# Kernel tuning notes

Measured on AMD Instinct MI355X. Metric: run time of the kernel, lower is better.

The kernel has to match this reference:

```python
import jax, jax.numpy as jnp
import numpy as np
import math

B, S, D, H = 2, 2048, 1024, 16
DK = D // H


def setup_inputs() -> dict:
    key = jax.random.key(0)
    ks = jax.random.split(key, 11)
    s = 1.0 / math.sqrt(D)
    return {
        "q": jax.random.normal(ks[0], (B, S, D), jnp.float32),
        "k": jax.random.normal(ks[1], (B, S, D), jnp.float32),
        "v": jax.random.normal(ks[2], (B, S, D), jnp.float32),
        "Wq": jax.random.normal(ks[3], (D, D), jnp.float32) * s,
        "bq": jnp.zeros((D,), jnp.float32),
        "Wk": jax.random.normal(ks[4], (D, D), jnp.float32) * s,
        "bk": jnp.zeros((D,), jnp.float32),
        "Wv": jax.random.normal(ks[5], (D, D), jnp.float32) * s,
        "bv": jnp.zeros((D,), jnp.float32),
        "Wo": jax.random.normal(ks[6], (D, D), jnp.float32) * s,
        "bo": jnp.zeros((D,), jnp.float32),
        "mask": jnp.ones((B, 1, S), dtype=bool),
    }


def reference(q, k, v, Wq, bq, Wk, bk, Wv, bv, Wo, bo, mask):
    # project and split heads: [B,S,D] -> [B,H,S,DK]
    def proj(x, W, b):
        return (x @ W.T + b).reshape(B, S, H, DK).transpose(0, 2, 1, 3)

    qh, kh, vh = proj(q, Wq, bq), proj(k, Wk, bk), proj(v, Wv, bv)
    scores = jnp.einsum("bhqd,bhkd->bhqk", qh, kh) / math.sqrt(DK)
    # 3D mask [B,1,S], self-attn: expand to [B,1,S,S] via outer AND
    m = mask[:, :, None, :] & mask[:, :, :, None]
    scores = jnp.where(m, scores, -1e9)
    attn = jax.nn.softmax(scores, axis=-1)
    attn = jnp.nan_to_num(attn, nan=0.0, posinf=0.0, neginf=0.0)
    out = jnp.einsum("bhqk,bhkd->bhqd", attn, vh)  # [B,H,S,DK]
    concat = out.transpose(0, 2, 1, 3).reshape(B, S, D)
    return concat @ Wo.T + bo
```

## Files before the change

### kernel.cpp

```cpp
#include <hip/hip_runtime.h>
#include <hip/hip_bf16.h>
#include <stdint.h>

using bf16 = __bf16;
typedef __attribute__((ext_vector_type(8))) __bf16 bf16x8;
typedef __attribute__((ext_vector_type(4))) float f32x4;

typedef const __attribute__((address_space(1))) void* gptr_t;
typedef __attribute__((address_space(3))) void* lptr_t;

__device__ __forceinline__ void gld16(const void* g, void* l) {
    __builtin_amdgcn_global_load_lds((gptr_t)g, (lptr_t)l, 16, 0, 0);
}

__global__ __launch_bounds__(256)
void cvt_kern(const float* __restrict__ in, bf16* __restrict__ out, int n)
{
    const int i = (blockIdx.x * 256 + threadIdx.x) * 8;
    if (i >= n) return;
    const float4 f0 = *(const float4*)(in + i);
    const float4 f1 = *(const float4*)(in + i + 4);
    bf16x8 v = { (bf16)f0.x, (bf16)f0.y, (bf16)f0.z, (bf16)f0.w,
                 (bf16)f1.x, (bf16)f1.y, (bf16)f1.z, (bf16)f1.w };
    *(bf16x8*)(out + i) = v;
}

template<int MODE, bool XWS, bool OUTF32>
__global__ __launch_bounds__(512, 2)
void gemm_mfma(const void* __restrict__ Xv, const bf16* __restrict__ W,
               const float* __restrict__ bias, void* __restrict__ Yv)
{
    constexpr int K = 1024, N = 1024;
    constexpr int NT = K / 64;
    __shared__ bf16 As[2][128 * 64];
    __shared__ bf16 Bs[2][128 * 64];

    const int t = threadIdx.x;
    const int w = t >> 6, lane = t & 63, quad = lane >> 4, l15 = lane & 15;
    const int m0 = blockIdx.y * 128, n0 = blockIdx.x * 128;
    const int wm = (w >> 1) * 32, wn = (w & 1) * 64;

    const int srow = t >> 3;
    const int sseg = (t & 7) ^ (srow & 7);

    const float* Xf   = (const float*)Xv;
    const bf16*  gA16 = (const bf16*)Xv + (size_t)(m0 + srow) * K + sseg * 8;
    const bf16*  gB   = W + (size_t)(n0 + srow) * K + sseg * 8;

    f32x4 acc[2][4] = {};

    if constexpr (XWS) {
        gld16(gA16,          &As[0][t * 8]);
        gld16(gA16 + 64 * K, &As[0][t * 8 + 4096]);
    } else {
        #pragma unroll
        for (int r = 0; r < 2; ++r) {
            const int g = r * 512 + t;
            const int row = g >> 3, sg = g & 7;
            const float* p = Xf + (size_t)(m0 + row) * K + sg * 8;
            const float4 f0 = *(const float4*)p;
            const float4 f1 = *(const float4*)(p + 4);
            bf16x8 vv = { (bf16)f0.x, (bf16)f0.y, (bf16)f0.z, (bf16)f0.w,
                          (bf16)f1.x, (bf16)f1.y, (bf16)f1.z, (bf16)f1.w };
            *(bf16x8*)&As[0][row * 64 + ((sg ^ (row & 7)) * 8)] = vv;
        }
    }
    gld16(gB,          &Bs[0][t * 8]);
    gld16(gB + 64 * K, &Bs[0][t * 8 + 4096]);
    __syncthreads();

    #pragma unroll 2
    for (int kk = 0; kk < NT; ++kk) {
        const int cur = kk & 1;
        const int kn = (kk + 1) * 64;

        float4 pf0[2], pf1[2];
        if (kk + 1 < NT) {
            if constexpr (XWS) {
                gld16(gA16 + kn,          &As[cur ^ 1][t * 8]);
                gld16(gA16 + kn + 64 * K, &As[cur ^ 1][t * 8 + 4096]);
            } else {
                #pragma unroll
                for (int r = 0; r < 2; ++r) {
                    const int g = r * 512 + t;
                    const int row = g >> 3, sg = g & 7;
                    const float* p = Xf + (size_t)(m0 + row) * K + kn + sg * 8;
                    pf0[r] = *(const float4*)p;
                    pf1[r] = *(const float4*)(p + 4);
                }
            }
            gld16(gB + kn,          &Bs[cur ^ 1][t * 8]);
            gld16(gB + kn + 64 * K, &Bs[cur ^ 1][t * 8 + 4096]);
        }

        bf16x8 af[2][2], bfr[4][2];
        #pragma unroll
        for (int mt = 0; mt < 2; ++mt)
            #pragma unroll
            for (int kt = 0; kt < 2; ++kt) {
                const int row = wm + mt * 16 + l15;
                const int seg = (kt * 4 + quad) ^ (row & 7);
                af[mt][kt] = *(const bf16x8*)&As[cur][row * 64 + seg * 8];
            }
        #pragma unroll
        for (int nt = 0; nt < 4; ++nt)
            #pragma unroll
            for (int kt = 0; kt < 2; ++kt) {
                const int row = wn + nt * 16 + l15;
                const int seg = (kt * 4 + quad) ^ (row & 7);
                bfr[nt][kt] = *(const bf16x8*)&Bs[cur][row * 64 + seg * 8];
            }
        #pragma unroll
        for (int kt = 0; kt < 2; ++kt)
            #pragma unroll
            for (int mt = 0; mt < 2; ++mt)
                #pragma unroll
                for (int nt = 0; nt < 4; ++nt)
                    acc[mt][nt] = __builtin_amdgcn_mfma_f32_16x16x32_bf16(
                        af[mt][kt], bfr[nt][kt], acc[mt][nt], 0, 0, 0);

        if (kk + 1 < NT) {
            if constexpr (!XWS) {
                #pragma unroll
                for (int r = 0; r < 2; ++r) {
                    const int g = r * 512 + t;
                    const int row = g >> 3, sg = g & 7;
                    bf16x8 vv = { (bf16)pf0[r].x, (bf16)pf0[r].y,
                                  (bf16)pf0[r].z, (bf16)pf0[r].w,
                                  (bf16)pf1[r].x, (bf16)pf1[r].y,
                                  (bf16)pf1[r].z, (bf16)pf1[r].w };
                    *(bf16x8*)&As[cur ^ 1][row * 64 + ((sg ^ (row & 7)) * 8)] = vv;
                }
            }
        }
        __syncthreads();
    }

    #pragma unroll
    for (int nt = 0; nt < 4; ++nt) {
        const int col = n0 + wn + nt * 16 + l15;
        const float bv = bias[col];
        #pragma unroll
        for (int mt = 0; mt < 2; ++mt)
            #pragma unroll
            for (int i = 0; i < 4; ++i) {
                const int row = m0 + wm + mt * 16 + quad * 4 + i;
                const float v = acc[mt][nt][i] + bv;
                if (MODE == 0) {
                    const size_t off = (size_t)row * N + col;
                    if (OUTF32) ((float*)Yv)[off] = v;
                    else        ((bf16*)Yv)[off]  = (bf16)v;
                } else {
                    const int b = row >> 11, s = row & 2047;
                    const int h = col >> 6, d = col & 63;
                    ((bf16*)Yv)[(((size_t)(b * 16 + h) * 64 + d) << 11) + s] = (bf16)v;
                }
            }
    }
}

__global__ __launch_bounds__(512, 4)
void attn_mfma(const bf16* __restrict__ Q, const bf16* __restrict__ Kg,
               const bf16* __restrict__ Vt, bf16* Cc)
{
    constexpr int S = 2048, D = 1024, DK = 64, LDP = 72;
    __shared__ bf16 Qs[128 * 64];
    __shared__ bf16 Ks[64 * 64];
    __shared__ bf16 Vs[80 * 64];
    __shared__ bf16 Ps[8][16 * LDP];

    const int t = threadIdx.x;
    const int w = t >> 6, lane = t & 63, quad = lane >> 4, l15 = lane & 15;
    const int bh = blockIdx.y, b = bh >> 4, h = bh & 15;
    const int q0 = blockIdx.x * 128;
    const int wq = w * 16;

    const int srow = t >> 3;
    const int sseg = (t & 7) ^ (srow & 7);

    for (int i = t; i < 16 * 64; i += 512) {
        const int r = 64 + (i >> 6);
        Vs[r * 64 + (i & 63)] = (r == 64) ? (bf16)1.0f : (bf16)0.0f;
    }

    {
        const bf16* gQ = Q + (size_t)(b * S + q0 + srow) * D + h * DK + sseg * 8;
        gld16(gQ,                  Qs + t * 8);
        gld16(gQ + (size_t)64 * D, Qs + t * 8 + 4096);
    }
    __syncthreads();

    bf16x8 aq[2];
    #pragma unroll
    for (int kt = 0; kt < 2; ++kt) {
        const int row = wq + l15;
        const int seg = (kt * 4 + quad) ^ (row & 7);
        aq[kt] = *(const bf16x8*)&Qs[row * 64 + seg * 8];
    }

    f32x4 o[5] = {};
    float mrow[4];
    #pragma unroll
    for (int i = 0; i < 4; ++i) mrow[i] = -1e30f;

    const float c = 0.125f * 1.44269504088896340736f;

    const bf16* gK = Kg + (size_t)(b * S + srow) * D + h * DK + sseg * 8;
    const bf16* gV = Vt + ((size_t)bh * DK + srow) * S + sseg * 8;

    for (int s0 = 0; s0 < S; s0 += 64) {
        gld16(gK + (size_t)s0 * D, Ks + t * 8);
        gld16(gV + s0,             Vs + t * 8);
        __syncthreads();

        f32x4 sa[4] = {};
        bf16x8 bk[4][2];
        #pragma unroll
        for (int nt = 0; nt < 4; ++nt)
            #pragma unroll
            for (int kt = 0; kt < 2; ++kt) {
                const int row = nt * 16 + l15;
                const int seg = (kt * 4 + quad) ^ (row & 7);
                bk[nt][kt] = *(const bf16x8*)&Ks[row * 64 + seg * 8];
            }
        #pragma unroll
        for (int kt = 0; kt < 2; ++kt)
            #pragma unroll
            for (int nt = 0; nt < 4; ++nt)
                sa[nt] = __builtin_amdgcn_mfma_f32_16x16x32_bf16(
                    aq[kt], bk[nt][kt], sa[nt], 0, 0, 0);

        #pragma unroll
        for (int i = 0; i < 4; ++i) {
            float v = fmaxf(fmaxf(sa[0][i], sa[1][i]),
                            fmaxf(sa[2][i], sa[3][i])) * c;
            v = fmaxf(v, __shfl_xor(v, 1));
            v = fmaxf(v, __shfl_xor(v, 2));
            v = fmaxf(v, __shfl_xor(v, 4));
            v = fmaxf(v, __shfl_xor(v, 8));
            if (__any(v > mrow[i] + 8.0f)) {
                const float mnew = fmaxf(mrow[i], v);
                const float alpha = __builtin_amdgcn_exp2f(mrow[i] - mnew);
                mrow[i] = mnew;
                #pragma unroll
                for (int nt = 0; nt < 5; ++nt)
                    o[nt][i] *= alpha;
            }
            const int prow = quad * 4 + i;
            #pragma unroll
            for (int nt = 0; nt < 4; ++nt) {
                const float pv = __builtin_amdgcn_exp2f(sa[nt][i] * c - mrow[i]);
                Ps[w][prow * LDP + nt * 16 + l15] = (bf16)pv;
            }
        }

        bf16x8 ap[2], bvv[5][2];
        #pragma unroll
        for (int kt = 0; kt < 2; ++kt)
            ap[kt] = *(const bf16x8*)&Ps[w][l15 * LDP + kt * 32 + quad * 8];
        #pragma unroll
        for (int nt = 0; nt < 5; ++nt)
            #pragma unroll
            for (int kt = 0; kt < 2; ++kt) {
                const int row = nt * 16 + l15;
                const int seg = (kt * 4 + quad) ^ (row & 7);
                bvv[nt][kt] = *(const bf16x8*)&Vs[row * 64 + seg * 8];
            }
        #pragma unroll
        for (int kt = 0; kt < 2; ++kt)
            #pragma unroll
            for (int nt = 0; nt < 5; ++nt)
                o[nt] = __builtin_amdgcn_mfma_f32_16x16x32_bf16(
                    ap[kt], bvv[nt][kt], o[nt], 0, 0, 0);

        __syncthreads();
    }

    #pragma unroll
    for (int i = 0; i < 4; ++i) {
        const int row = q0 + wq + quad * 4 + i;
        const float lsum = __shfl(o[4][i], quad << 4);
        const float inv = 1.0f / lsum;
        #pragma unroll
        for (int nt = 0; nt < 4; ++nt) {
            const int col = nt * 16 + l15;
            Cc[(size_t)(b * S + row) * D + h * DK + col] = (bf16)(o[nt][i] * inv);
        }
    }
}

extern "C" void kernel_launch(void* const* d_in, const int* in_sizes, int n_in,
                              void* d_out, int out_size, void* d_ws, size_t ws_size,
                              hipStream_t stream)
{
    int iq=0, ik=1, iv=2, iWq=3, ibq=4, iWk=5, ibk=6, iWv=7, ibv=8, iWo=9, ibo=10;
    if (n_in >= 12 && in_sizes[0] == 1048576) {
        iWk=0; iWo=1; iWq=2; iWv=3; ibk=4; ibo=5; ibq=6; ibv=7; ik=8; iq=10; iv=11;
    }

    const float* q  = (const float*)d_in[iq];
    const float* k  = (const float*)d_in[ik];
    const float* v  = (const float*)d_in[iv];
    const float* Wq = (const float*)d_in[iWq];
    const float* bq = (const float*)d_in[ibq];
    const float* Wk = (const float*)d_in[iWk];
    const float* bk = (const float*)d_in[ibk];
    const float* Wv = (const float*)d_in[iWv];
    const float* bv = (const float*)d_in[ibv];
    const float* Wo = (const float*)d_in[iWo];
    const float* bo = (const float*)d_in[ibo];

    bf16* Qp  = (bf16*)d_ws;
    bf16* Kp  = Qp  + (size_t)4194304;
    bf16* Vtp = Kp  + (size_t)4194304;
    bf16* Wqb = Vtp + (size_t)4194304;
    bf16* Wkb = Wqb + (size_t)1048576;
    bf16* Wvb = Wkb + (size_t)1048576;
    bf16* Wob = Wvb + (size_t)1048576;
    bf16* qb  = Wob + (size_t)1048576;
    bf16* kb  = qb  + (size_t)4194304;
    bf16* vb  = kb  + (size_t)4194304;
    bf16* Cc  = Qp;

    constexpr int WN = 1048576, XN = 4194304;
    cvt_kern<<<WN / 2048, 256, 0, stream>>>(Wq, Wqb, WN);
    cvt_kern<<<WN / 2048, 256, 0, stream>>>(Wk, Wkb, WN);
    cvt_kern<<<WN / 2048, 256, 0, stream>>>(Wv, Wvb, WN);
    cvt_kern<<<WN / 2048, 256, 0, stream>>>(Wo, Wob, WN);

    const bool pre = ws_size >= (size_t)56 * 1024 * 1024;
    dim3 gg(8, 32), bb(512);
    if (pre) {
        cvt_kern<<<XN / 2048, 256, 0, stream>>>(q, qb, XN);
        cvt_kern<<<XN / 2048, 256, 0, stream>>>(k, kb, XN);
        cvt_kern<<<XN / 2048, 256, 0, stream>>>(v, vb, XN);
        gemm_mfma<0, true, false><<<gg, bb, 0, stream>>>(qb, Wqb, bq, Qp);
        gemm_mfma<0, true, false><<<gg, bb, 0, stream>>>(kb, Wkb, bk, Kp);
        gemm_mfma<1, true, false><<<gg, bb, 0, stream>>>(vb, Wvb, bv, Vtp);
    } else {
        gemm_mfma<0, false, false><<<gg, bb, 0, stream>>>(q, Wqb, bq, Qp);
        gemm_mfma<0, false, false><<<gg, bb, 0, stream>>>(k, Wkb, bk, Kp);
        gemm_mfma<1, false, false><<<gg, bb, 0, stream>>>(v, Wvb, bv, Vtp);
    }
    attn_mfma<<<dim3(16, 32), dim3(512), 0, stream>>>(Qp, Kp, Vtp, Cc);
    gemm_mfma<0, true, true><<<gg, bb, 0, stream>>>(Cc, Wob, bo, d_out);
}
```

Measured before the change: 286.4 us.

## Rewrite bf16 GEMM with 256-thread blocks, 4x4 warp tiles and vmcnt-based pipelining

Replaces the bf16-input GEMM with a 256-thread variant in which each wave computes a 64x64 tile, so the same 128x128 block tile is covered by fewer waves with more MFMA work each. Tiles are prefetched two stages ahead with direct-to-LDS loads, and explicit s_waitcnt vmcnt plus raw barriers take the place of __syncthreads, letting loads stay in flight across iterations. Input conversion reuses a single bf16 scratch buffer interleaved with each projection, which lowers the workspace threshold for the precision-converted path. The cost is higher register pressure from 16 accumulator tiles per wave and fragile manual wait counts.

```diff
diff --git a/kernel.cpp b/kernel.cpp
--- a/kernel.cpp
+++ b/kernel.cpp
@@ -25,77 +25,51 @@
     *(bf16x8*)(out + i) = v;
 }
 
-template<int MODE, bool XWS, bool OUTF32>
-__global__ __launch_bounds__(512, 2)
-void gemm_mfma(const void* __restrict__ Xv, const bf16* __restrict__ W,
-               const float* __restrict__ bias, void* __restrict__ Yv)
+template<int MODE, bool OUTF32>
+__global__ __launch_bounds__(256, 2)
+void gemm_cnt(const bf16* __restrict__ X, const bf16* __restrict__ W,
+              const float* __restrict__ bias, void* __restrict__ Yv)
 {
-    constexpr int K = 1024, N = 1024;
-    constexpr int NT = K / 64;
+    constexpr int K = 1024, N = 1024, NT = K / 64;
     __shared__ bf16 As[2][128 * 64];
     __shared__ bf16 Bs[2][128 * 64];
 
     const int t = threadIdx.x;
     const int w = t >> 6, lane = t & 63, quad = lane >> 4, l15 = lane & 15;
     const int m0 = blockIdx.y * 128, n0 = blockIdx.x * 128;
-    const int wm = (w >> 1) * 32, wn = (w & 1) * 64;
+    const int wm = (w >> 1) * 64, wn = (w & 1) * 64;
 
     const int srow = t >> 3;
     const int sseg = (t & 7) ^ (srow & 7);
 
-    const float* Xf   = (const float*)Xv;
-    const bf16*  gA16 = (const bf16*)Xv + (size_t)(m0 + srow) * K + sseg * 8;
-    const bf16*  gB   = W + (size_t)(n0 + srow) * K + sseg * 8;
-
-    f32x4 acc[2][4] = {};
-
-    if constexpr (XWS) {
-        gld16(gA16,          &As[0][t * 8]);
-        gld16(gA16 + 64 * K, &As[0][t * 8 + 4096]);
-    } else {
-        #pragma unroll
-        for (int r = 0; r < 2; ++r) {
-            const int g = r * 512 + t;
-            const int row = g >> 3, sg = g & 7;
-            const float* p = Xf + (size_t)(m0 + row) * K + sg * 8;
-            const float4 f0 = *(const float4*)p;
-            const float4 f1 = *(const float4*)(p + 4);
-            bf16x8 vv = { (bf16)f0.x, (bf16)f0.y, (bf16)f0.z, (bf16)f0.w,
-                          (bf16)f1.x, (bf16)f1.y, (bf16)f1.z, (bf16)f1.w };
-            *(bf16x8*)&As[0][row * 64 + ((sg ^ (row & 7)) * 8)] = vv;
-        }
-    }
-    gld16(gB,          &Bs[0][t * 8]);
-    gld16(gB + 64 * K, &Bs[0][t * 8 + 4096]);
-    __syncthreads();
-
-    #pragma unroll 2
+    const bf16* gA = X + (size_t)(m0 + srow) * K + sseg * 8;
+    const bf16* gB = W + (size_t)(n0 + srow) * K + sseg * 8;
+
+    auto stage = [&](int buf, int k0) {
+        #pragma unroll
+        for (int r = 0; r < 4; ++r)
+            gld16(gA + k0 + r * 32 * K, &As[buf][t * 8 + r * 2048]);
+        #pragma unroll
+        for (int r = 0; r < 4; ++r)
+            gld16(gB + k0 + r * 32 * K, &Bs[buf][t * 8 + r * 2048]);
+    };
+
+    stage(0, 0);
+    stage(1, 64);
+
+    f32x4 acc[4][4] = {};
+
+    #pragma unroll 1
     for (int kk = 0; kk < NT; ++kk) {
         const int cur = kk & 1;
-        const int kn = (kk + 1) * 64;
-
-        float4 pf0[2], pf1[2];
-        if (kk + 1 < NT) {
-            if constexpr (XWS) {
-                gld16(gA16 + kn,          &As[cur ^ 1][t * 8]);
-                gld16(gA16 + kn + 64 * K, &As[cur ^ 1][t * 8 + 4096]);
-            } else {
-                #pragma unroll
-                for (int r = 0; r < 2; ++r) {
-                    const int g = r * 512 + t;
-                    const int row = g >> 3, sg = g & 7;
-                    const float* p = Xf + (size_t)(m0 + row) * K + kn + sg * 8;
-                    pf0[r] = *(const float4*)p;
-                    pf1[r] = *(const float4*)(p + 4);
-                }
-            }
-            gld16(gB + kn,          &Bs[cur ^ 1][t * 8]);
-            gld16(gB + kn + 64 * K, &Bs[cur ^ 1][t * 8 + 4096]);
-        }
-
-        bf16x8 af[2][2], bfr[4][2];
-        #pragma unroll
-        for (int mt = 0; mt < 2; ++mt)
+        if (kk == NT - 1) asm volatile("s_waitcnt vmcnt(0)" ::: "memory");
+        else              asm volatile("s_waitcnt vmcnt(8)" ::: "memory");
+        __builtin_amdgcn_s_barrier();
+        asm volatile("" ::: "memory");
+
+        bf16x8 af[4][2], bfr[4][2];
+        #pragma unroll
+        for (int mt = 0; mt < 4; ++mt)
             #pragma unroll
             for (int kt = 0; kt < 2; ++kt) {
                 const int row = wm + mt * 16 + l15;
@@ -113,27 +87,16 @@
         #pragma unroll
         for (int kt = 0; kt < 2; ++kt)
             #pragma unroll
-            for (int mt = 0; mt < 2; ++mt)
+            for (int mt = 0; mt < 4; ++mt)
                 #pragma unroll
                 for (int nt = 0; nt < 4; ++nt)
                     acc[mt][nt] = __builtin_amdgcn_mfma_f32_16x16x32_bf16(
                         af[mt][kt], bfr[nt][kt], acc[mt][nt], 0, 0, 0);
 
-        if (kk + 1 < NT) {
-            if constexpr (!XWS) {
-                #pragma unroll
-                for (int r = 0; r < 2; ++r) {
-                    const int g = r * 512 + t;
-                    const int row = g >> 3, sg = g & 7;
-                    bf16x8 vv = { (bf16)pf0[r].x, (bf16)pf0[r].y,
-                                  (bf16)pf0[r].z, (bf16)pf0[r].w,
-                                  (bf16)pf1[r].x, (bf16)pf1[r].y,
-                                  (bf16)pf1[r].z, (bf16)pf1[r].w };
-                    *(bf16x8*)&As[cur ^ 1][row * 64 + ((sg ^ (row & 7)) * 8)] = vv;
-                }
-            }
-        }
-        __syncthreads();
+        asm volatile("" ::: "memory");
+        __builtin_amdgcn_s_barrier();
+        asm volatile("" ::: "memory");
+        if (kk + 2 < NT) stage(cur, (kk + 2) * 64);
     }
 
     #pragma unroll
@@ -141,7 +104,7 @@
         const int col = n0 + wn + nt * 16 + l15;
         const float bv = bias[col];
         #pragma unroll
-        for (int mt = 0; mt < 2; ++mt)
+        for (int mt = 0; mt < 4; ++mt)
             #pragma unroll
             for (int i = 0; i < 4; ++i) {
                 const int row = m0 + wm + mt * 16 + quad * 4 + i;
@@ -150,6 +113,123 @@
                     const size_t off = (size_t)row * N + col;
                     if (OUTF32) ((float*)Yv)[off] = v;
                     else        ((bf16*)Yv)[off]  = (bf16)v;
+                } else {
+                    const int b = row >> 11, s = row & 2047;
+                    const int h = col >> 6, d = col & 63;
+                    ((bf16*)Yv)[(((size_t)(b * 16 + h) * 64 + d) << 11) + s] = (bf16)v;
+                }
+            }
+    }
+}
+
+template<int MODE>
+__global__ __launch_bounds__(512, 2)
+void gemm_f32(const float* __restrict__ Xf, const bf16* __restrict__ W,
+              const float* __restrict__ bias, void* __restrict__ Yv)
+{
+    constexpr int K = 1024, N = 1024;
+    constexpr int NT = K / 64;
+    __shared__ bf16 As[2][128 * 64];
+    __shared__ bf16 Bs[2][128 * 64];
+
+    const int t = threadIdx.x;
+    const int w = t >> 6, lane = t & 63, quad = lane >> 4, l15 = lane & 15;
+    const int m0 = blockIdx.y * 128, n0 = blockIdx.x * 128;
+    const int wm = (w >> 1) * 32, wn = (w & 1) * 64;
+
+    const int srow = t >> 3;
+    const int sseg = (t & 7) ^ (srow & 7);
+
+    const bf16* gB = W + (size_t)(n0 + srow) * K + sseg * 8;
+
+    f32x4 acc[2][4] = {};
+
+    #pragma unroll
+    for (int r = 0; r < 2; ++r) {
+        const int g = r * 512 + t;
+        const int row = g >> 3, sg = g & 7;
+        const float* p = Xf + (size_t)(m0 + row) * K + sg * 8;
+        const float4 f0 = *(const float4*)p;
+        const float4 f1 = *(const float4*)(p + 4);
+        bf16x8 vv = { (bf16)f0.x, (bf16)f0.y, (bf16)f0.z, (bf16)f0.w,
+                      (bf16)f1.x, (bf16)f1.y, (bf16)f1.z, (bf16)f1.w };
+        *(bf16x8*)&As[0][row * 64 + ((sg ^ (row & 7)) * 8)] = vv;
+    }
+    gld16(gB,          &Bs[0][t * 8]);
+    gld16(gB + 64 * K, &Bs[0][t * 8 + 4096]);
+    __syncthreads();
+
+    for (int kk = 0; kk < NT; ++kk) {
+        const int cur = kk & 1;
+        const int kn = (kk + 1) * 64;
+
+        float4 pf0[2], pf1[2];
+        if (kk + 1 < NT) {
+            #pragma unroll
+            for (int r = 0; r < 2; ++r) {
+                const int g = r * 512 + t;
+                const int row = g >> 3, sg = g & 7;
+                const float* p = Xf + (size_t)(m0 + row) * K + kn + sg * 8;
+                pf0[r] = *(const float4*)p;
+                pf1[r] = *(const float4*)(p + 4);
+            }
+            gld16(gB + kn,          &Bs[cur ^ 1][t * 8]);
+            gld16(gB + kn + 64 * K, &Bs[cur ^ 1][t * 8 + 4096]);
+        }
+
+        bf16x8 af[2][2], bfr[4][2];
+        #pragma unroll
+        for (int mt = 0; mt < 2; ++mt)
+            #pragma unroll
+            for (int kt = 0; kt < 2; ++kt) {
+                const int row = wm + mt * 16 + l15;
+                const int seg = (kt * 4 + quad) ^ (row & 7);
+                af[mt][kt] = *(const bf16x8*)&As[cur][row * 64 + seg * 8];
+            }
+        #pragma unroll
+        for (int nt = 0; nt < 4; ++nt)
+            #pragma unroll
+            for (int kt = 0; kt < 2; ++kt) {
+                const int row = wn + nt * 16 + l15;
+                const int seg = (kt * 4 + quad) ^ (row & 7);
+                bfr[nt][kt] = *(const bf16x8*)&Bs[cur][row * 64 + seg * 8];
+            }
+        #pragma unroll
+        for (int kt = 0; kt < 2; ++kt)
+            #pragma unroll
+            for (int mt = 0; mt < 2; ++mt)
+                #pragma unroll
+                for (int nt = 0; nt < 4; ++nt)
+                    acc[mt][nt] = __builtin_amdgcn_mfma_f32_16x16x32_bf16(
+                        af[mt][kt], bfr[nt][kt], acc[mt][nt], 0, 0, 0);
+
+        if (kk + 1 < NT) {
+            #pragma unroll
+            for (int r = 0; r < 2; ++r) {
+                const int g = r * 512 + t;
+                const int row = g >> 3, sg = g & 7;
+                bf16x8 vv = { (bf16)pf0[r].x, (bf16)pf0[r].y,
+                              (bf16)pf0[r].z, (bf16)pf0[r].w,
+                              (bf16)pf1[r].x, (bf16)pf1[r].y,
+                              (bf16)pf1[r].z, (bf16)pf1[r].w };
+                *(bf16x8*)&As[cur ^ 1][row * 64 + ((sg ^ (row & 7)) * 8)] = vv;
+            }
+        }
+        __syncthreads();
+    }
+
+    #pragma unroll
+    for (int nt = 0; nt < 4; ++nt) {
+        const int col = n0 + wn + nt * 16 + l15;
+        const float bv = bias[col];
+        #pragma unroll
+        for (int mt = 0; mt < 2; ++mt)
+            #pragma unroll
+            for (int i = 0; i < 4; ++i) {
+                const int row = m0 + wm + mt * 16 + quad * 4 + i;
+                const float v = acc[mt][nt][i] + bv;
+                if (MODE == 0) {
+                    ((bf16*)Yv)[(size_t)row * N + col] = (bf16)v;
                 } else {
                     const int b = row >> 11, s = row & 2047;
                     const int h = col >> 6, d = col & 63;
@@ -317,9 +397,7 @@
     bf16* Wkb = Wqb + (size_t)1048576;
     bf16* Wvb = Wkb + (size_t)1048576;
     bf16* Wob = Wvb + (size_t)1048576;
-    bf16* qb  = Wob + (size_t)1048576;
-    bf16* kb  = qb  + (size_t)4194304;
-    bf16* vb  = kb  + (size_t)4194304;
+    bf16* xb  = Wob + (size_t)1048576;
     bf16* Cc  = Qp;
 
     constexpr int WN = 1048576, XN = 4194304;
@@ -328,20 +406,20 @@
     cvt_kern<<<WN / 2048, 256, 0, stream>>>(Wv, Wvb, WN);
     cvt_kern<<<WN / 2048, 256, 0, stream>>>(Wo, Wob, WN);
 
-    const bool pre = ws_size >= (size_t)56 * 1024 * 1024;
-    dim3 gg(8, 32), bb(512);
+    const bool pre = ws_size >= (size_t)40 * 1024 * 1024;
+    dim3 gg(8, 32);
     if (pre) {
-        cvt_kern<<<XN / 2048, 256, 0, stream>>>(q, qb, XN);
-        cvt_kern<<<XN / 2048, 256, 0, stream>>>(k, kb, XN);
-        cvt_kern<<<XN / 2048, 256, 0, stream>>>(v, vb, XN);
-        gemm_mfma<0, true, false><<<gg, bb, 0, stream>>>(qb, Wqb, bq, Qp);
-        gemm_mfma<0, true, false><<<gg, bb, 0, stream>>>(kb, Wkb, bk, Kp);
-        gemm_mfma<1, true, false><<<gg, bb, 0, stream>>>(vb, Wvb, bv, Vtp);
+        cvt_kern<<<XN / 2048, 256, 0, stream>>>(q, xb, XN);
+        gemm_cnt<0, false><<<gg, dim3(256), 0, stream>>>(xb, Wqb, bq, Qp);
+        cvt_kern<<<XN / 2048, 256, 0, stream>>>(k, xb, XN);
+        gemm_cnt<0, false><<<gg, dim3(256), 0, stream>>>(xb, Wkb, bk, Kp);
+        cvt_kern<<<XN / 2048, 256, 0, stream>>>(v, xb, XN);
+        gemm_cnt<1, false><<<gg, dim3(256), 0, stream>>>(xb, Wvb, bv, Vtp);
     } else {
-        gemm_mfma<0, false, false><<<gg, bb, 0, stream>>>(q, Wqb, bq, Qp);
-        gemm_mfma<0, false, false><<<gg, bb, 0, stream>>>(k, Wkb, bk, Kp);
-        gemm_mfma<1, false, false><<<gg, bb, 0, stream>>>(v, Wvb, bv, Vtp);
+        gemm_f32<0><<<gg, dim3(512), 0, stream>>>(q, Wqb, bq, Qp);
+        gemm_f32<0><<<gg, dim3(512), 0, stream>>>(k, Wkb, bk, Kp);
+        gemm_f32<1><<<gg, dim3(512), 0, stream>>>(v, Wvb, bv, Vtp);
     }
     attn_mfma<<<dim3(16, 32), dim3(512), 0, stream>>>(Qp, Kp, Vtp, Cc);
-    gemm_mfma<0, true, true><<<gg, bb, 0, stream>>>(Cc, Wob, bo, d_out);
-}
+    gemm_cnt<0, true><<<gg, dim3(256), 0, stream>>>(Cc, Wob, bo, d_out);
+}
```

New measurement: 298.4 us. 4.2% more time.
